# Performance work log

Measured on AMD Instinct MI355X. Metric: run time of the kernel, lower is better.

Reference implementation:

```python
import jax, jax.numpy as jnp
import numpy as np

OBS = 128; N_AGENT = 16; N_ACTION = 8; N_LAYER = 2; HID = 128
GE = 256; LE = 256; F1 = 512; F2 = 512


def _edges(batch_size, n):
    # all ordered pairs (i, j), i != j, within each sample; GCNConv adds self-loops
    i, j = np.meshgrid(np.arange(n), np.arange(n), indexing='ij')
    m = i != j
    src0, dst0 = i[m], j[m]                      # [n*(n-1)]
    off = (np.arange(batch_size) * n)[:, None]
    src = (src0[None, :] + off).reshape(-1)
    dst = (dst0[None, :] + off).reshape(-1)
    return jnp.asarray(src, jnp.int32), jnp.asarray(dst, jnp.int32)


def setup_inputs() -> dict:
    key = jax.random.key(0)
    ks = jax.random.split(key, 16)
    g = lambda k, shp, fan: jax.random.normal(k, shp, jnp.float32) / np.sqrt(fan)
    return {
        'obs_j': jax.random.normal(ks[0], (2048, N_AGENT, OBS), jnp.float32),
        'W_pre': g(ks[1], (OBS, HID), OBS), 'b_pre': jnp.zeros((HID,), jnp.float32),
        'W_gcn': g(ks[2], (N_LAYER, HID, HID), HID), 'b_gcn': jnp.zeros((N_LAYER, HID), jnp.float32),
        'W_post': g(ks[3], (HID, GE), HID), 'b_post': jnp.zeros((GE,), jnp.float32),
        'W_loc': g(ks[4], (OBS, LE), OBS), 'b_loc': jnp.zeros((LE,), jnp.float32),
        'W1': g(ks[5], (GE + LE, F1), GE + LE), 'b1': jnp.zeros((F1,), jnp.float32),
        'W2': g(ks[6], (F1, F2), F1), 'b2': jnp.zeros((F2,), jnp.float32),
        'W3': g(ks[7], (F2, N_ACTION), F2), 'b3': jnp.zeros((N_ACTION,), jnp.float32),
    }


def reference(obs_j, W_pre, b_pre, W_gcn, b_gcn, W_post, b_post,
              W_loc, b_loc, W1, b1, W2, b2, W3, b3):
    B, n, _ = obs_j.shape
    N = B * n
    obs = obs_j.reshape(N, OBS)
    x = jax.nn.relu(obs @ W_pre + b_pre)          # [N, HID]

    src, dst = _edges(B, n)
    # GCNConv with self-loops on a fully-connected graph: deg = n for every node,
    # edge norm = 1/sqrt(deg_i*deg_j) = 1/n for every (A+I) edge.
    inv_n = jnp.float32(1.0) / n
    for l in range(N_LAYER):
        h = x @ W_gcn[l]                          # lin (no bias inside propagate)
        agg = jax.ops.segment_sum(h[src], dst, num_segments=N)  # neighbor gather/scatter
        x = jax.nn.relu((agg + h) * inv_n + b_gcn[l])            # + self-loop msg, bias

    g = x.reshape(B, n, HID).mean(axis=1)         # global_mean_pool over each graph
    g = jax.nn.relu(g @ W_post + b_post)          # [B, GE]
    loc = jax.nn.relu(obs @ W_loc + b_loc)        # [B*n, LE]
    gi = jnp.repeat(g, n, axis=0)                 # repeat_interleave over agents
    z = jnp.concatenate([gi, loc], axis=1)
    z = jax.nn.relu(z @ W1 + b1)
    z = jax.nn.relu(z @ W2 + b2)
    q = z @ W3 + b3
    return q.reshape(B, n, N_ACTION)
```

## Files before the change

### kernel.cpp

```cpp
#include <hip/hip_runtime.h>
#include <hip/hip_bf16.h>
#include <stdint.h>

typedef __bf16 bf16;
typedef __bf16 bf16x4 __attribute__((ext_vector_type(4)));
typedef __bf16 bf16x8 __attribute__((ext_vector_type(8)));
typedef float f32x4 __attribute__((ext_vector_type(4)));

#define MFMA(a, b, c) __builtin_amdgcn_mfma_f32_16x16x32_bf16(a, b, c, 0, 0, 0)
#define GL(p) ((const __attribute__((address_space(1))) void*)(p))
#define SH(p) ((__attribute__((address_space(3))) void*)(p))

__device__ inline void tp(const float* W, bf16* WT, int id, int shiftK, int N) {
  int K = 1 << shiftK;
  int n = id >> shiftK;
  int k = id & (K - 1);
  WT[id] = (bf16)W[(size_t)k * N + n];
}

__global__ __launch_bounds__(256) void prep_all(
    const float* __restrict__ W1, const float* __restrict__ W2,
    bf16* __restrict__ W1T, bf16* __restrict__ W2T,
    const float* __restrict__ Wpre, const float* __restrict__ Wloc,
    const float* __restrict__ Wgcn, const float* __restrict__ Wpost,
    bf16* __restrict__ WpreLocT, bf16* __restrict__ Wg0T, bf16* __restrict__ Wg1T,
    bf16* __restrict__ WpostT,
    const float* __restrict__ bpre, const float* __restrict__ bloc,
    float* __restrict__ biasPL,
    const float* __restrict__ W3, bf16* __restrict__ W3bT,
    float* __restrict__ outq) {
  __shared__ bf16 tile[64 * 68];
  int blk = blockIdx.x;
  int tid = threadIdx.x;
  if (blk < 128) {
    const float* W = (blk < 64) ? W1 : W2;
    bf16* WT = (blk < 64) ? W1T : W2T;
    int t = blk & 63;
    int tk0 = (t >> 3) * 64, tn0 = (t & 7) * 64;
#pragma unroll
    for (int p = 0; p < 4; p++) {
      int kr = p * 16 + (tid >> 4), nc = (tid & 15) * 4;
      float4 f = *(const float4*)(W + (size_t)(tk0 + kr) * 512 + tn0 + nc);
      bf16x4 v; v[0] = (bf16)f.x; v[1] = (bf16)f.y; v[2] = (bf16)f.z; v[3] = (bf16)f.w;
      *(bf16x4*)&tile[kr * 68 + nc] = v;
    }
    __syncthreads();
#pragma unroll
    for (int p = 0; p < 4; p++) {
      int nr = p * 16 + (tid >> 4), kc = (tid & 15) * 4;
      bf16x4 v;
#pragma unroll
      for (int i = 0; i < 4; i++) v[i] = tile[(kc + i) * 68 + nr];
      *(bf16x4*)(WT + (size_t)(tn0 + nr) * 512 + tk0 + kc) = v;
    }
    return;
  }
  blk -= 128;
  if (blk < 448) {
    int id = blk * 256 + tid;
    if (id < 16384) { tp(Wpre, WpreLocT, id, 7, 128); return; } id -= 16384;
    if (id < 32768) { tp(Wloc, WpreLocT + 16384, id, 7, 256); return; } id -= 32768;
    if (id < 16384) { tp(Wgcn, Wg0T, id, 7, 128); return; } id -= 16384;
    if (id < 16384) { tp(Wgcn + 16384, Wg1T, id, 7, 128); return; } id -= 16384;
    tp(Wpost, WpostT, id, 7, 256);
    return;
  }
  blk -= 448;
  if (blk == 0) {
    if (tid < 128) biasPL[tid] = bpre[tid];
    biasPL[128 + tid] = bloc[tid];
    return;
  }
  blk -= 1;
  if (blk == 0) {
#pragma unroll
    for (int i = 0; i < 32; i++) {
      int id = i * 256 + tid;
      int n = id >> 9, k = id & 511;
      float w = (n < 8) ? W3[(size_t)k * 8 + n] : 0.f;
      bf16 hi = (bf16)w;
      W3bT[id] = hi;
      W3bT[8192 + id] = (bf16)(w - (float)hi);
    }
    return;
  }
  blk -= 1;
  float4 z = {0.f, 0.f, 0.f, 0.f};
#pragma unroll
  for (int i = 0; i < 4; i++)
    ((float4*)outq)[(size_t)blk * 1024 + i * 256 + tid] = z;
}

__global__ __launch_bounds__(256, 4) void k1c(
    const float* __restrict__ obs, const bf16* __restrict__ WpreLocT,
    const float* __restrict__ biasPL,
    const bf16* __restrict__ Wg0T, const bf16* __restrict__ Wg1T,
    const bf16* __restrict__ WpostT, const float* __restrict__ b_gcn,
    const float* __restrict__ b_post,
    const bf16* __restrict__ W1T, const float* __restrict__ b1,
    bf16* __restrict__ loc, float* __restrict__ h) {
  __shared__ bf16 smem[16384];

  const int tid = threadIdx.x;
  const int id = blockIdx.x;
  const int s = id >> 3;
  const int n_idx = s % 3;
  const int m0 = ((id & 7) + 8 * (s / 3)) * 128;
  const int n0 = n_idx * 128;

  f32x4 acc[4][4] = {};
  const int lane = tid & 63, wave = tid >> 6;
  const int wm = (wave >> 1) * 64, wn = (wave & 1) * 64;
  const int lm = lane & 15, quad = lane >> 4;

  float4 pa[4];

  auto loadA = [&](int kt) {
#pragma unroll
    for (int it = 0; it < 2; it++) {
      int idx = it * 256 + tid;
      int row = idx >> 2;
      int c = idx & 3;
      int cv = c ^ ((row >> 1) & 3);
      const float* src = obs + (size_t)(m0 + row) * 128 + kt * 32 + cv * 8;
      pa[it * 2] = *(const float4*)src;
      pa[it * 2 + 1] = *(const float4*)(src + 4);
    }
  };
  auto stageB = [&](int kt, int buf) {
    bf16* Bd = smem + buf * 8192 + 4096;
#pragma unroll
    for (int it = 0; it < 2; it++) {
      int idx = it * 256 + tid;
      int row = idx >> 2;
      int c = idx & 3;
      int cv = c ^ ((row >> 1) & 3);
      const bf16* gb = WpreLocT + (size_t)(n0 + row) * 128 + kt * 32 + cv * 8;
      __builtin_amdgcn_global_load_lds(GL(gb), SH(&Bd[(idx & ~63) * 8]), 16, 0, 0);
    }
  };
  auto commitA = [&](int buf) {
    bf16* Ad = smem + buf * 8192;
#pragma unroll
    for (int it = 0; it < 2; it++) {
      int idx = it * 256 + tid;
      int row = idx >> 2;
      int c = idx & 3;
      float4 f0 = pa[it * 2], f1 = pa[it * 2 + 1];
      bf16x8 v;
      v[0] = (bf16)f0.x; v[1] = (bf16)f0.y; v[2] = (bf16)f0.z; v[3] = (bf16)f0.w;
      v[4] = (bf16)f1.x; v[5] = (bf16)f1.y; v[6] = (bf16)f1.z; v[7] = (bf16)f1.w;
      *(bf16x8*)&Ad[row * 32 + c * 8] = v;
    }
  };
  auto compute = [&](int buf) {
    const bf16* Ar = smem + buf * 8192;
    const bf16* Br = smem + buf * 8192 + 4096;
    bf16x8 a[4], b[4];
#pragma unroll
    for (int i = 0; i < 4; i++) {
      int r = wm + lm + i * 16;
      a[i] = *(const bf16x8*)&Ar[r * 32 + ((quad ^ ((r >> 1) & 3)) * 8)];
    }
#pragma unroll
    for (int j = 0; j < 4; j++) {
      int r = wn + lm + j * 16;
      b[j] = *(const bf16x8*)&Br[r * 32 + ((quad ^ ((r >> 1) & 3)) * 8)];
    }
#pragma unroll
    for (int i = 0; i < 4; i++)
#pragma unroll
      for (int j = 0; j < 4; j++)
        acc[i][j] = MFMA(a[i], b[j], acc[i][j]);
  };

  loadA(0); stageB(0, 0); commitA(0);
  __syncthreads();
#pragma unroll
  for (int i = 0; i < 4; ++i) {
    if (i + 1 < 4) { loadA(i + 1); stageB(i + 1, (i + 1) & 1); }
    compute(i & 1);
    if (i + 1 < 4) commitA((i + 1) & 1);
    __syncthreads();
  }

  if (n_idx == 0) {
    bf16* xs = smem;
    bf16* x2 = smem + 2176;
    bf16* gS = smem + 4352;
#pragma unroll
    for (int i = 0; i < 4; i++) {
      int sl = (wave >> 1) * 4 + i;
#pragma unroll
      for (int j = 0; j < 4; j++) {
        int col = wn + j * 16 + lm;
        float bb = biasPL[col];
        float v = 0.f;
#pragma unroll
        for (int r = 0; r < 4; r++) v += fmaxf(acc[i][j][r] + bb, 0.f);
        v += __shfl_xor(v, 16);
        v += __shfl_xor(v, 32);
        if (quad == 0) xs[sl * 136 + col] = (bf16)(v * 0.0625f);
        else if (quad == 1) xs[(8 + sl) * 136 + col] = (bf16)0.f;
      }
    }
    __syncthreads();
    {
      f32x4 c2[2] = {};
#pragma unroll
      for (int ku = 0; ku < 4; ++ku) {
        bf16x8 a = *(const bf16x8*)&xs[lm * 136 + (ku * 4 + quad) * 8];
#pragma unroll
        for (int jn = 0; jn < 2; ++jn) {
          int col = (wave * 2 + jn) * 16 + lm;
          bf16x8 b = *(const bf16x8*)&Wg0T[(size_t)col * 128 + ku * 32 + quad * 8];
          c2[jn] = MFMA(a, b, c2[jn]);
        }
      }
      __syncthreads();
#pragma unroll
      for (int jn = 0; jn < 2; ++jn) {
        int col = (wave * 2 + jn) * 16 + lm;
        float bb = b_gcn[col];
#pragma unroll
        for (int r = 0; r < 4; ++r)
          x2[(quad * 4 + r) * 136 + col] = (bf16)fmaxf(c2[jn][r] + bb, 0.f);
      }
    }
    __syncthreads();
    {
      f32x4 c2[2] = {};
#pragma unroll
      for (int ku = 0; ku < 4; ++ku) {
        bf16x8 a = *(const bf16x8*)&x2[lm * 136 + (ku * 4 + quad) * 8];
#pragma unroll
        for (int jn = 0; jn < 2; ++jn) {
          int col = (wave * 2 + jn) * 16 + lm;
          bf16x8 b = *(const bf16x8*)&Wg1T[(size_t)col * 128 + ku * 32 + quad * 8];
          c2[jn] = MFMA(a, b, c2[jn]);
        }
      }
      __syncthreads();
#pragma unroll
      for (int jn = 0; jn < 2; ++jn) {
        int col = (wave * 2 + jn) * 16 + lm;
        float bb = b_gcn[128 + col];
#pragma unroll
        for (int r = 0; r < 4; ++r)
          xs[(quad * 4 + r) * 136 + col] = (bf16)fmaxf(c2[jn][r] + bb, 0.f);
      }
    }
    __syncthreads();
    {
      f32x4 c3[4] = {};
#pragma unroll
      for (int ku = 0; ku < 4; ++ku) {
        bf16x8 a = *(const bf16x8*)&xs[lm * 136 + (ku * 4 + quad) * 8];
#pragma unroll
        for (int jn = 0; jn < 4; ++jn) {
          int col = (wave * 4 + jn) * 16 + lm;
          bf16x8 b = *(const bf16x8*)&WpostT[(size_t)col * 128 + ku * 32 + quad * 8];
          c3[jn] = MFMA(a, b, c3[jn]);
        }
      }
#pragma unroll
      for (int jn = 0; jn < 4; ++jn) {
        int col = (wave * 4 + jn) * 16 + lm;
        float bb = b_post[col];
#pragma unroll
        for (int r = 0; r < 4; ++r)
          gS[(quad * 4 + r) * 264 + col] = (bf16)fmaxf(c3[jn][r] + bb, 0.f);
      }
    }
    __syncthreads();
    {
      f32x4 hacc[8] = {};
#pragma unroll
      for (int ku = 0; ku < 8; ++ku) {
        bf16x8 a = *(const bf16x8*)&gS[lm * 264 + ku * 32 + quad * 8];
#pragma unroll
        for (int jn = 0; jn < 8; ++jn) {
          int col = (wave * 8 + jn) * 16 + lm;
          bf16x8 b = *(const bf16x8*)&W1T[(size_t)col * 512 + ku * 32 + quad * 8];
          hacc[jn] = MFMA(a, b, hacc[jn]);
        }
      }
      int sample0 = m0 >> 4;
#pragma unroll
      for (int jn = 0; jn < 8; ++jn) {
        int col = (wave * 8 + jn) * 16 + lm;
        float bb = b1[col];
#pragma unroll
        for (int r = 0; r < 4; ++r) {
          int row = quad * 4 + r;
          if (row < 8)
            h[(size_t)(sample0 + row) * 512 + col] = hacc[jn][r] + bb;
        }
      }
    }
  } else {
#pragma unroll
    for (int i = 0; i < 4; i++)
#pragma unroll
      for (int j = 0; j < 4; j++) {
        int col = wn + j * 16 + lm;
        float bb = biasPL[n0 + col];
#pragma unroll
        for (int r = 0; r < 4; r++) {
          int row = wm + i * 16 + quad * 4 + r;
          smem[row * 128 + col] = (bf16)fmaxf(acc[i][j][r] + bb, 0.f);
        }
      }
    __syncthreads();
    const int coff = n0 - 128;
#pragma unroll
    for (int c = 0; c < 8; c++) {
      int ci = c * 256 + tid;
      int row = ci >> 4, col8 = (ci & 15) * 8;
      *(bf16x8*)&loc[(size_t)(m0 + row) * 256 + coff + col8] = *(const bf16x8*)&smem[row * 128 + col8];
    }
  }
}

template <bool HREP>
__global__ __launch_bounds__(256, 4) void gemm_k(
    const bf16* __restrict__ Ab, const bf16* __restrict__ BT,
    const float* __restrict__ bias, const float* __restrict__ hrep,
    bf16* __restrict__ C,
    const bf16* __restrict__ W3bT, const float* __restrict__ b3,
    float* __restrict__ outq) {
  __shared__ bf16 smem[16384];

  const int tid = threadIdx.x;
  const int id = blockIdx.x;
  const int s = id >> 3;
  const int n_idx = s & 3;
  const int m0 = ((id & 7) + 8 * (s >> 2)) * 128;
  const int n0 = n_idx * 128;

  f32x4 acc[4][4] = {};
  const int lane = tid & 63, wave = tid >> 6;
  const int wm = (wave >> 1) * 64, wn = (wave & 1) * 64;
  const int lm = lane & 15, quad = lane >> 4;

  auto stage = [&](int kt, int buf) {
    bf16* Ad = smem + buf * 8192;
    bf16* Bd = smem + buf * 8192 + 4096;
    int k0 = kt * 32;
#pragma unroll
    for (int it = 0; it < 2; it++) {
      int idx = it * 256 + tid;
      int row = idx >> 2;
      int c = idx & 3;
      int cv = c ^ ((row >> 1) & 3);
      int kk = k0 + cv * 8;
      const bf16* ga = HREP ? (Ab + (size_t)(m0 + row) * 256 + kk)
                            : (Ab + (size_t)(m0 + row) * 512 + kk);
      __builtin_amdgcn_global_load_lds(GL(ga), SH(&Ad[(idx & ~63) * 8]), 16, 0, 0);
      const bf16* gb = HREP ? (BT + (size_t)(n0 + row) * 512 + 256 + kk)
                            : (BT + (size_t)(n0 + row) * 512 + kk);
      __builtin_amdgcn_global_load_lds(GL(gb), SH(&Bd[(idx & ~63) * 8]), 16, 0, 0);
    }
  };

  auto compute = [&](int buf) {
    const bf16* Ar = smem + buf * 8192;
    const bf16* Br = smem + buf * 8192 + 4096;
    bf16x8 a[4], b[4];
#pragma unroll
    for (int i = 0; i < 4; i++) {
      int r = wm + lm + i * 16;
      a[i] = *(const bf16x8*)&Ar[r * 32 + ((quad ^ ((r >> 1) & 3)) * 8)];
    }
#pragma unroll
    for (int j = 0; j < 4; j++) {
      int r = wn + lm + j * 16;
      b[j] = *(const bf16x8*)&Br[r * 32 + ((quad ^ ((r >> 1) & 3)) * 8)];
    }
#pragma unroll
    for (int i = 0; i < 4; i++)
#pragma unroll
      for (int j = 0; j < 4; j++)
        acc[i][j] = MFMA(a[i], b[j], acc[i][j]);
  };

  const int NIT = HREP ? 8 : 16;
  stage(0, 0);
  __syncthreads();
#pragma unroll 2
  for (int i = 0; i < NIT; ++i) {
    if (i + 1 < NIT) stage(i + 1, (i + 1) & 1);
    compute(i & 1);
    __syncthreads();
  }

  if (HREP) {
#pragma unroll
    for (int i = 0; i < 4; i++) {
      int sample = (m0 + wm + i * 16) >> 4;
#pragma unroll
      for (int j = 0; j < 4; j++) {
        int col = n0 + wn + j * 16 + lm;
        float hv = hrep[(size_t)sample * 512 + col];
#pragma unroll
        for (int r = 0; r < 4; r++) {
          int row = wm + i * 16 + quad * 4 + r;
          smem[row * 128 + (col - n0)] = (bf16)fmaxf(acc[i][j][r] + hv, 0.f);
        }
      }
    }
    __syncthreads();
#pragma unroll
    for (int c = 0; c < 8; c++) {
      int ci = c * 256 + tid;
      int row = ci >> 4, col8 = (ci & 15) * 8;
      *(bf16x8*)&C[(size_t)(m0 + row) * 512 + n0 + col8] = *(const bf16x8*)&smem[row * 128 + col8];
    }
  } else {
#pragma unroll
    for (int i = 0; i < 4; i++)
#pragma unroll
      for (int j = 0; j < 4; j++) {
        int col = wn + j * 16 + lm;
        float bb = bias[n0 + col];
#pragma unroll
        for (int r = 0; r < 4; r++) {
          int row = wm + i * 16 + quad * 4 + r;
          int pc = (col >> 3) ^ (row & 7);
          smem[row * 128 + pc * 8 + (col & 7)] = (bf16)fmaxf(acc[i][j][r] + bb, 0.f);
        }
      }
    __syncthreads();
    bf16x8 w3h[4], w3l[4];
#pragma unroll
    for (int kt = 0; kt < 4; kt++) {
      w3h[kt] = *(const bf16x8*)&W3bT[lm * 512 + n0 + kt * 32 + quad * 8];
      w3l[kt] = *(const bf16x8*)&W3bT[8192 + lm * 512 + n0 + kt * 32 + quad * 8];
    }
    f32x4 qacc[2] = {};
#pragma unroll
    for (int it = 0; it < 2; it++)
#pragma unroll
      for (int kt = 0; kt < 4; kt++) {
        int rr = wave * 32 + it * 16 + lm;
        bf16x8 a = *(const bf16x8*)&smem[rr * 128 + (((kt * 4 + quad) ^ (rr & 7)) * 8)];
        qacc[it] = MFMA(a, w3h[kt], qacc[it]);
        qacc[it] = MFMA(a, w3l[kt], qacc[it]);
      }
    float qb = (n_idx == 0 && lm < 8) ? b3[lm] : 0.f;
    if (lm < 8) {
#pragma unroll
      for (int it = 0; it < 2; it++)
#pragma unroll
        for (int r = 0; r < 4; r++) {
          int row = m0 + wave * 32 + it * 16 + quad * 4 + r;
          atomicAdd(&outq[(size_t)row * 8 + lm], qacc[it][r] + qb);
        }
    }
  }
}

extern "C" void kernel_launch(void* const* d_in, const int* in_sizes, int n_in,
                              void* d_out, int out_size, void* d_ws, size_t ws_size,
                              hipStream_t stream) {
  const float* obs    = (const float*)d_in[0];
  const float* W_pre  = (const float*)d_in[1];
  const float* b_pre  = (const float*)d_in[2];
  const float* W_gcn  = (const float*)d_in[3];
  const float* b_gcn  = (const float*)d_in[4];
  const float* W_post = (const float*)d_in[5];
  const float* b_post = (const float*)d_in[6];
  const float* W_loc  = (const float*)d_in[7];
  const float* b_loc  = (const float*)d_in[8];
  const float* W1     = (const float*)d_in[9];
  const float* b1     = (const float*)d_in[10];
  const float* W2     = (const float*)d_in[11];
  const float* b2     = (const float*)d_in[12];
  const float* W3     = (const float*)d_in[13];
  const float* b3     = (const float*)d_in[14];
  float* out = (float*)d_out;

  char* p = (char*)d_ws;
  auto alloc = [&](size_t bytes) { char* r = p; p += (bytes + 255) & ~(size_t)255; return r; };
  bf16* WpreLocT = (bf16*)alloc(384 * 128 * 2);
  float* biasPL  = (float*)alloc(384 * 4);
  bf16* Wg0T   = (bf16*)alloc(128 * 128 * 2);
  bf16* Wg1T   = (bf16*)alloc(128 * 128 * 2);
  bf16* WpostT = (bf16*)alloc(256 * 128 * 2);
  bf16* W1T    = (bf16*)alloc(512 * 512 * 2);
  bf16* W2T    = (bf16*)alloc(512 * 512 * 2);
  bf16* W3bT   = (bf16*)alloc(2 * 16 * 512 * 2);
  bf16* locB   = (bf16*)alloc((size_t)32768 * 256 * 2);
  float* hB    = (float*)alloc((size_t)2048 * 512 * 4);
  bf16* z1B    = (bf16*)alloc((size_t)32768 * 512 * 2);

  prep_all<<<642, 256, 0, stream>>>(W1, W2, W1T, W2T,
                                    W_pre, W_loc, W_gcn, W_post,
                                    WpreLocT, Wg0T, Wg1T, WpostT,
                                    b_pre, b_loc, biasPL, W3, W3bT, out);
  k1c<<<768, 256, 0, stream>>>(obs, WpreLocT, biasPL,
                               Wg0T, Wg1T, WpostT, b_gcn, b_post,
                               W1T, b1, locB, hB);
  gemm_k<true><<<1024, 256, 0, stream>>>(locB, W1T, nullptr, hB, z1B,
                                         nullptr, nullptr, nullptr);
  gemm_k<false><<<1024, 256, 0, stream>>>(z1B, W2T, b2, nullptr, nullptr,
                                          W3bT, b3, out);
}
```

Measured before the change: 156.3 us.

## Enlarge GEMM tiles to 256x256 with 512-thread blocks and two-phase epilogue

The two large GEMM kernels move from 128x128 tiles on 256-thread blocks to 256x256 tiles on 512-thread blocks, each wave computing a 128x64 sub-tile. Doubling the tile in both dimensions halves the global loads per FLOP and gives more MFMAs per LDS fetch. Because LDS cannot hold the whole output tile, the epilogue runs in two halves with extra barriers. The grid drops from 1024 to 256 blocks, which is close to one wave of blocks on 256 CUs, and the doubled accumulators raise register pressure.

```diff
diff --git a/kernel.cpp b/kernel.cpp
--- a/kernel.cpp
+++ b/kernel.cpp
@@ -323,33 +323,32 @@
 }
 
 template <bool HREP>
-__global__ __launch_bounds__(256, 4) void gemm_k(
+__global__ __launch_bounds__(512, 2) void gemm_k(
     const bf16* __restrict__ Ab, const bf16* __restrict__ BT,
     const float* __restrict__ bias, const float* __restrict__ hrep,
     bf16* __restrict__ C,
     const bf16* __restrict__ W3bT, const float* __restrict__ b3,
     float* __restrict__ outq) {
-  __shared__ bf16 smem[16384];
+  __shared__ bf16 smem[32768];
 
   const int tid = threadIdx.x;
   const int id = blockIdx.x;
-  const int s = id >> 3;
-  const int n_idx = s & 3;
-  const int m0 = ((id & 7) + 8 * (s >> 2)) * 128;
-  const int n0 = n_idx * 128;
-
-  f32x4 acc[4][4] = {};
+  const int n_idx = id >> 7;
+  const int m0 = (id & 127) * 256;
+  const int n0 = n_idx * 256;
+
+  f32x4 acc[8][4] = {};
   const int lane = tid & 63, wave = tid >> 6;
-  const int wm = (wave >> 1) * 64, wn = (wave & 1) * 64;
+  const int wm = (wave >> 2) * 128, wn = (wave & 3) * 64;
   const int lm = lane & 15, quad = lane >> 4;
 
   auto stage = [&](int kt, int buf) {
-    bf16* Ad = smem + buf * 8192;
-    bf16* Bd = smem + buf * 8192 + 4096;
+    bf16* Ad = smem + buf * 16384;
+    bf16* Bd = smem + buf * 16384 + 8192;
     int k0 = kt * 32;
 #pragma unroll
     for (int it = 0; it < 2; it++) {
-      int idx = it * 256 + tid;
+      int idx = it * 512 + tid;
       int row = idx >> 2;
       int c = idx & 3;
       int cv = c ^ ((row >> 1) & 3);
@@ -364,11 +363,11 @@
   };
 
   auto compute = [&](int buf) {
-    const bf16* Ar = smem + buf * 8192;
-    const bf16* Br = smem + buf * 8192 + 4096;
-    bf16x8 a[4], b[4];
-#pragma unroll
-    for (int i = 0; i < 4; i++) {
+    const bf16* Ar = smem + buf * 16384;
+    const bf16* Br = smem + buf * 16384 + 8192;
+    bf16x8 a[8], b[4];
+#pragma unroll
+    for (int i = 0; i < 8; i++) {
       int r = wm + lm + i * 16;
       a[i] = *(const bf16x8*)&Ar[r * 32 + ((quad ^ ((r >> 1) & 3)) * 8)];
     }
@@ -378,7 +377,7 @@
       b[j] = *(const bf16x8*)&Br[r * 32 + ((quad ^ ((r >> 1) & 3)) * 8)];
     }
 #pragma unroll
-    for (int i = 0; i < 4; i++)
+    for (int i = 0; i < 8; i++)
 #pragma unroll
       for (int j = 0; j < 4; j++)
         acc[i][j] = MFMA(a[i], b[j], acc[i][j]);
@@ -396,57 +395,73 @@
 
   if (HREP) {
 #pragma unroll
-    for (int i = 0; i < 4; i++) {
-      int sample = (m0 + wm + i * 16) >> 4;
-#pragma unroll
-      for (int j = 0; j < 4; j++) {
-        int col = n0 + wn + j * 16 + lm;
-        float hv = hrep[(size_t)sample * 512 + col];
-#pragma unroll
-        for (int r = 0; r < 4; r++) {
-          int row = wm + i * 16 + quad * 4 + r;
-          smem[row * 128 + (col - n0)] = (bf16)fmaxf(acc[i][j][r] + hv, 0.f);
-        }
-      }
-    }
-    __syncthreads();
-#pragma unroll
-    for (int c = 0; c < 8; c++) {
-      int ci = c * 256 + tid;
-      int row = ci >> 4, col8 = (ci & 15) * 8;
-      *(bf16x8*)&C[(size_t)(m0 + row) * 512 + n0 + col8] = *(const bf16x8*)&smem[row * 128 + col8];
+    for (int h = 0; h < 2; ++h) {
+      if (h) __syncthreads();
+      if ((wave >> 2) == h) {
+#pragma unroll
+        for (int i = 0; i < 8; i++) {
+          int sample = (m0 + h * 128 + i * 16) >> 4;
+#pragma unroll
+          for (int j = 0; j < 4; j++) {
+            int col = (wave & 3) * 64 + j * 16 + lm;
+            float hv = hrep[(size_t)sample * 512 + n0 + col];
+#pragma unroll
+            for (int r = 0; r < 4; r++) {
+              int rl = i * 16 + quad * 4 + r;
+              smem[rl * 256 + col] = (bf16)fmaxf(acc[i][j][r] + hv, 0.f);
+            }
+          }
+        }
+      }
+      __syncthreads();
+#pragma unroll
+      for (int c = 0; c < 8; c++) {
+        int ci = c * 512 + tid;
+        int row = ci >> 5, col8 = (ci & 31) * 8;
+        *(bf16x8*)&C[(size_t)(m0 + h * 128 + row) * 512 + n0 + col8] =
+            *(const bf16x8*)&smem[row * 256 + col8];
+      }
     }
   } else {
-#pragma unroll
-    for (int i = 0; i < 4; i++)
-#pragma unroll
-      for (int j = 0; j < 4; j++) {
-        int col = wn + j * 16 + lm;
-        float bb = bias[n0 + col];
-#pragma unroll
-        for (int r = 0; r < 4; r++) {
-          int row = wm + i * 16 + quad * 4 + r;
-          int pc = (col >> 3) ^ (row & 7);
-          smem[row * 128 + pc * 8 + (col & 7)] = (bf16)fmaxf(acc[i][j][r] + bb, 0.f);
-        }
-      }
-    __syncthreads();
-    bf16x8 w3h[4], w3l[4];
-#pragma unroll
-    for (int kt = 0; kt < 4; kt++) {
+    bf16x8 w3h[8], w3l[8];
+#pragma unroll
+    for (int kt = 0; kt < 8; kt++) {
       w3h[kt] = *(const bf16x8*)&W3bT[lm * 512 + n0 + kt * 32 + quad * 8];
       w3l[kt] = *(const bf16x8*)&W3bT[8192 + lm * 512 + n0 + kt * 32 + quad * 8];
     }
     f32x4 qacc[2] = {};
 #pragma unroll
-    for (int it = 0; it < 2; it++)
-#pragma unroll
-      for (int kt = 0; kt < 4; kt++) {
-        int rr = wave * 32 + it * 16 + lm;
-        bf16x8 a = *(const bf16x8*)&smem[rr * 128 + (((kt * 4 + quad) ^ (rr & 7)) * 8)];
-        qacc[it] = MFMA(a, w3h[kt], qacc[it]);
-        qacc[it] = MFMA(a, w3l[kt], qacc[it]);
-      }
+    for (int h = 0; h < 2; ++h) {
+      if (h) __syncthreads();
+      if ((wave >> 2) == h) {
+#pragma unroll
+        for (int i = 0; i < 8; i++)
+#pragma unroll
+          for (int j = 0; j < 4; j++) {
+            int col = (wave & 3) * 64 + j * 16 + lm;
+            float bb = bias[n0 + col];
+#pragma unroll
+            for (int r = 0; r < 4; r++) {
+              int rl = i * 16 + quad * 4 + r;
+              int pc = (col >> 3) ^ (rl & 7);
+              smem[rl * 256 + pc * 8 + (col & 7)] = (bf16)fmaxf(acc[i][j][r] + bb, 0.f);
+            }
+          }
+      }
+      __syncthreads();
+      if ((wave >> 2) == h) {
+#pragma unroll
+        for (int it = 0; it < 2; it++) {
+          int rl = (wave & 3) * 32 + it * 16 + lm;
+#pragma unroll
+          for (int kt = 0; kt < 8; kt++) {
+            bf16x8 a = *(const bf16x8*)&smem[rl * 256 + (((kt * 4 + quad) ^ (rl & 7)) * 8)];
+            qacc[it] = MFMA(a, w3h[kt], qacc[it]);
+            qacc[it] = MFMA(a, w3l[kt], qacc[it]);
+          }
+        }
+      }
+    }
     float qb = (n_idx == 0 && lm < 8) ? b3[lm] : 0.f;
     if (lm < 8) {
 #pragma unroll
@@ -501,8 +516,8 @@
   k1c<<<768, 256, 0, stream>>>(obs, WpreLocT, biasPL,
                                Wg0T, Wg1T, WpostT, b_gcn, b_post,
                                W1T, b1, locB, hB);
-  gemm_k<true><<<1024, 256, 0, stream>>>(locB, W1T, nullptr, hB, z1B,
-                                         nullptr, nullptr, nullptr);
-  gemm_k<false><<<1024, 256, 0, stream>>>(z1B, W2T, b2, nullptr, nullptr,
-                                          W3bT, b3, out);
+  gemm_k<true><<<256, 512, 0, stream>>>(locB, W1T, nullptr, hB, z1B,
+                                        nullptr, nullptr, nullptr);
+  gemm_k<false><<<256, 512, 0, stream>>>(z1B, W2T, b2, nullptr, nullptr,
+                                         W3bT, b3, out);
 }
```

After: 163.9 us. +4.9%, slower.

## Move g@W1 projection into first MLP GEMM; shift W1/W2 prep into k1c

Applied to the files above, without the earlier changes.

The global embedding projection g@W1[:256]+b1 moves out of k1c, which now only writes g as bf16. The first MLP GEMM recomputes it per block into shared memory with a few extra MFMAs. The W1/W2 transposes, the W3 split and output zeroing move from prep_all into extra k1c blocks, so they overlap with k1c work and take load off the prep kernel's critical path. The cost is redundant h computation in every GEMM block (each sample's row is recomputed across column tiles) and more shared memory per block.

```diff
diff --git a/kernel.cpp b/kernel.cpp
--- a/kernel.cpp
+++ b/kernel.cpp
@@ -19,43 +19,14 @@
 }
 
 __global__ __launch_bounds__(256) void prep_all(
-    const float* __restrict__ W1, const float* __restrict__ W2,
-    bf16* __restrict__ W1T, bf16* __restrict__ W2T,
     const float* __restrict__ Wpre, const float* __restrict__ Wloc,
     const float* __restrict__ Wgcn, const float* __restrict__ Wpost,
     bf16* __restrict__ WpreLocT, bf16* __restrict__ Wg0T, bf16* __restrict__ Wg1T,
     bf16* __restrict__ WpostT,
     const float* __restrict__ bpre, const float* __restrict__ bloc,
-    float* __restrict__ biasPL,
-    const float* __restrict__ W3, bf16* __restrict__ W3bT,
-    float* __restrict__ outq) {
-  __shared__ bf16 tile[64 * 68];
+    float* __restrict__ biasPL) {
   int blk = blockIdx.x;
   int tid = threadIdx.x;
-  if (blk < 128) {
-    const float* W = (blk < 64) ? W1 : W2;
-    bf16* WT = (blk < 64) ? W1T : W2T;
-    int t = blk & 63;
-    int tk0 = (t >> 3) * 64, tn0 = (t & 7) * 64;
-#pragma unroll
-    for (int p = 0; p < 4; p++) {
-      int kr = p * 16 + (tid >> 4), nc = (tid & 15) * 4;
-      float4 f = *(const float4*)(W + (size_t)(tk0 + kr) * 512 + tn0 + nc);
-      bf16x4 v; v[0] = (bf16)f.x; v[1] = (bf16)f.y; v[2] = (bf16)f.z; v[3] = (bf16)f.w;
-      *(bf16x4*)&tile[kr * 68 + nc] = v;
-    }
-    __syncthreads();
-#pragma unroll
-    for (int p = 0; p < 4; p++) {
-      int nr = p * 16 + (tid >> 4), kc = (tid & 15) * 4;
-      bf16x4 v;
-#pragma unroll
-      for (int i = 0; i < 4; i++) v[i] = tile[(kc + i) * 68 + nr];
-      *(bf16x4*)(WT + (size_t)(tn0 + nr) * 512 + tk0 + kc) = v;
-    }
-    return;
-  }
-  blk -= 128;
   if (blk < 448) {
     int id = blk * 256 + tid;
     if (id < 16384) { tp(Wpre, WpreLocT, id, 7, 128); return; } id -= 16384;
@@ -65,30 +36,8 @@
     tp(Wpost, WpostT, id, 7, 256);
     return;
   }
-  blk -= 448;
-  if (blk == 0) {
-    if (tid < 128) biasPL[tid] = bpre[tid];
-    biasPL[128 + tid] = bloc[tid];
-    return;
-  }
-  blk -= 1;
-  if (blk == 0) {
-#pragma unroll
-    for (int i = 0; i < 32; i++) {
-      int id = i * 256 + tid;
-      int n = id >> 9, k = id & 511;
-      float w = (n < 8) ? W3[(size_t)k * 8 + n] : 0.f;
-      bf16 hi = (bf16)w;
-      W3bT[id] = hi;
-      W3bT[8192 + id] = (bf16)(w - (float)hi);
-    }
-    return;
-  }
-  blk -= 1;
-  float4 z = {0.f, 0.f, 0.f, 0.f};
-#pragma unroll
-  for (int i = 0; i < 4; i++)
-    ((float4*)outq)[(size_t)blk * 1024 + i * 256 + tid] = z;
+  if (tid < 128) biasPL[tid] = bpre[tid];
+  biasPL[128 + tid] = bloc[tid];
 }
 
 __global__ __launch_bounds__(256, 4) void k1c(
@@ -97,12 +46,63 @@
     const bf16* __restrict__ Wg0T, const bf16* __restrict__ Wg1T,
     const bf16* __restrict__ WpostT, const float* __restrict__ b_gcn,
     const float* __restrict__ b_post,
-    const bf16* __restrict__ W1T, const float* __restrict__ b1,
-    bf16* __restrict__ loc, float* __restrict__ h) {
+    bf16* __restrict__ gB, bf16* __restrict__ loc,
+    const float* __restrict__ W1, const float* __restrict__ W2,
+    bf16* __restrict__ W1T, bf16* __restrict__ W2T,
+    const float* __restrict__ W3, bf16* __restrict__ W3bT,
+    float* __restrict__ outq) {
   __shared__ bf16 smem[16384];
 
   const int tid = threadIdx.x;
-  const int id = blockIdx.x;
+  int id = blockIdx.x;
+
+  if (id >= 768) {
+    int blk = id - 768;
+    if (blk < 128) {
+      bf16* tile = smem;
+      const float* W = (blk < 64) ? W1 : W2;
+      bf16* WT = (blk < 64) ? W1T : W2T;
+      int t = blk & 63;
+      int tk0 = (t >> 3) * 64, tn0 = (t & 7) * 64;
+#pragma unroll
+      for (int p = 0; p < 4; p++) {
+        int kr = p * 16 + (tid >> 4), nc = (tid & 15) * 4;
+        float4 f = *(const float4*)(W + (size_t)(tk0 + kr) * 512 + tn0 + nc);
+        bf16x4 v; v[0] = (bf16)f.x; v[1] = (bf16)f.y; v[2] = (bf16)f.z; v[3] = (bf16)f.w;
+        *(bf16x4*)&tile[kr * 68 + nc] = v;
+      }
+      __syncthreads();
+#pragma unroll
+      for (int p = 0; p < 4; p++) {
+        int nr = p * 16 + (tid >> 4), kc = (tid & 15) * 4;
+        bf16x4 v;
+#pragma unroll
+        for (int i = 0; i < 4; i++) v[i] = tile[(kc + i) * 68 + nr];
+        *(bf16x4*)(WT + (size_t)(tn0 + nr) * 512 + tk0 + kc) = v;
+      }
+      return;
+    }
+    blk -= 128;
+    if (blk == 0) {
+#pragma unroll
+      for (int i = 0; i < 32; i++) {
+        int id2 = i * 256 + tid;
+        int n = id2 >> 9, k = id2 & 511;
+        float w = (n < 8) ? W3[(size_t)k * 8 + n] : 0.f;
+        bf16 hi = (bf16)w;
+        W3bT[id2] = hi;
+        W3bT[8192 + id2] = (bf16)(w - (float)hi);
+      }
+      return;
+    }
+    blk -= 1;
+    float4 z = {0.f, 0.f, 0.f, 0.f};
+#pragma unroll
+    for (int i = 0; i < 4; i++)
+      ((float4*)outq)[(size_t)blk * 1024 + i * 256 + tid] = z;
+    return;
+  }
+
   const int s = id >> 3;
   const int n_idx = s % 3;
   const int m0 = ((id & 7) + 8 * (s / 3)) * 128;
@@ -274,29 +274,10 @@
     }
     __syncthreads();
     {
-      f32x4 hacc[8] = {};
-#pragma unroll
-      for (int ku = 0; ku < 8; ++ku) {
-        bf16x8 a = *(const bf16x8*)&gS[lm * 264 + ku * 32 + quad * 8];
-#pragma unroll
-        for (int jn = 0; jn < 8; ++jn) {
-          int col = (wave * 8 + jn) * 16 + lm;
-          bf16x8 b = *(const bf16x8*)&W1T[(size_t)col * 512 + ku * 32 + quad * 8];
-          hacc[jn] = MFMA(a, b, hacc[jn]);
-        }
-      }
       int sample0 = m0 >> 4;
-#pragma unroll
-      for (int jn = 0; jn < 8; ++jn) {
-        int col = (wave * 8 + jn) * 16 + lm;
-        float bb = b1[col];
-#pragma unroll
-        for (int r = 0; r < 4; ++r) {
-          int row = quad * 4 + r;
-          if (row < 8)
-            h[(size_t)(sample0 + row) * 512 + col] = hacc[jn][r] + bb;
-        }
-      }
+      int row = tid >> 5, col8 = (tid & 31) * 8;
+      *(bf16x8*)&gB[(size_t)(sample0 + row) * 256 + col8] =
+          *(const bf16x8*)&gS[row * 264 + col8];
     }
   } else {
 #pragma unroll
@@ -325,11 +306,12 @@
 template <bool HREP>
 __global__ __launch_bounds__(256, 4) void gemm_k(
     const bf16* __restrict__ Ab, const bf16* __restrict__ BT,
-    const float* __restrict__ bias, const float* __restrict__ hrep,
+    const float* __restrict__ bias, const bf16* __restrict__ gB2,
     bf16* __restrict__ C,
     const bf16* __restrict__ W3bT, const float* __restrict__ b3,
     float* __restrict__ outq) {
-  __shared__ bf16 smem[16384];
+  __shared__ bf16 smem[18432];
+  float* const h_s = (float*)(smem + 16384);
 
   const int tid = threadIdx.x;
   const int id = blockIdx.x;
@@ -395,17 +377,42 @@
   }
 
   if (HREP) {
+    {
+      f32x4 hacc[2] = {};
+      int sample0 = m0 >> 4;
+      int arow = sample0 + lm;
+      if (arow > 2047) arow = 2047;
+#pragma unroll
+      for (int ku = 0; ku < 8; ++ku) {
+        bf16x8 a = *(const bf16x8*)&gB2[(size_t)arow * 256 + ku * 32 + quad * 8];
+#pragma unroll
+        for (int jn = 0; jn < 2; ++jn) {
+          int col = n0 + (wave * 2 + jn) * 16 + lm;
+          bf16x8 b = *(const bf16x8*)&BT[(size_t)col * 512 + ku * 32 + quad * 8];
+          hacc[jn] = MFMA(a, b, hacc[jn]);
+        }
+      }
+      if (quad < 2) {
+#pragma unroll
+        for (int jn = 0; jn < 2; ++jn) {
+          int colr = (wave * 2 + jn) * 16 + lm;
+#pragma unroll
+          for (int r = 0; r < 4; ++r)
+            h_s[(quad * 4 + r) * 128 + colr] = hacc[jn][r] + bias[n0 + colr];
+        }
+      }
+    }
+    __syncthreads();
 #pragma unroll
     for (int i = 0; i < 4; i++) {
-      int sample = (m0 + wm + i * 16) >> 4;
+      int rl = (wm >> 4) + i;
 #pragma unroll
       for (int j = 0; j < 4; j++) {
-        int col = n0 + wn + j * 16 + lm;
-        float hv = hrep[(size_t)sample * 512 + col];
+        float hv = h_s[rl * 128 + wn + j * 16 + lm];
 #pragma unroll
         for (int r = 0; r < 4; r++) {
           int row = wm + i * 16 + quad * 4 + r;
-          smem[row * 128 + (col - n0)] = (bf16)fmaxf(acc[i][j][r] + hv, 0.f);
+          smem[row * 128 + wn + j * 16 + lm] = (bf16)fmaxf(acc[i][j][r] + hv, 0.f);
         }
       }
     }
@@ -490,18 +497,18 @@
   bf16* W1T    = (bf16*)alloc(512 * 512 * 2);
   bf16* W2T    = (bf16*)alloc(512 * 512 * 2);
   bf16* W3bT   = (bf16*)alloc(2 * 16 * 512 * 2);
+  bf16* gB     = (bf16*)alloc((size_t)2048 * 256 * 2);
   bf16* locB   = (bf16*)alloc((size_t)32768 * 256 * 2);
-  float* hB    = (float*)alloc((size_t)2048 * 512 * 4);
   bf16* z1B    = (bf16*)alloc((size_t)32768 * 512 * 2);
 
-  prep_all<<<642, 256, 0, stream>>>(W1, W2, W1T, W2T,
-                                    W_pre, W_loc, W_gcn, W_post,
+  prep_all<<<449, 256, 0, stream>>>(W_pre, W_loc, W_gcn, W_post,
                                     WpreLocT, Wg0T, Wg1T, WpostT,
-                                    b_pre, b_loc, biasPL, W3, W3bT, out);
-  k1c<<<768, 256, 0, stream>>>(obs, WpreLocT, biasPL,
+                                    b_pre, b_loc, biasPL);
+  k1c<<<961, 256, 0, stream>>>(obs, WpreLocT, biasPL,
                                Wg0T, Wg1T, WpostT, b_gcn, b_post,
-                               W1T, b1, locB, hB);
-  gemm_k<true><<<1024, 256, 0, stream>>>(locB, W1T, nullptr, hB, z1B,
+                               gB, locB,
+                               W1, W2, W1T, W2T, W3, W3bT, out);
+  gemm_k<true><<<1024, 256, 0, stream>>>(locB, W1T, b1, gB, z1B,
                                          nullptr, nullptr, nullptr);
   gemm_k<false><<<1024, 256, 0, stream>>>(z1B, W2T, b2, nullptr, nullptr,
                                           W3bT, b3, out);
```

After: 153.3 us. Within noise of the previous version (-1.9%).
